# Kernel optimization log

Hardware: AMD Instinct MI355X
Metric: run time of the kernel (lower is better)

## Reference

```python
import jax, jax.numpy as jnp
import numpy as np
import math

NUM_HEADS = 16
SIZE = 1024
HEAD_SIZE = SIZE // NUM_HEADS
B, S = 2, 2048


def setup_inputs() -> dict:
    key = jax.random.key(0)
    ks = jax.random.split(key, 11)
    sc = 1.0 / math.sqrt(SIZE)
    inp = {
        "q": jax.random.normal(ks[0], (B, S, SIZE), dtype=jnp.float32),
        "k": jax.random.normal(ks[1], (B, S, SIZE), dtype=jnp.float32),
        "v": jax.random.normal(ks[2], (B, S, SIZE), dtype=jnp.float32),
        "Wq": jax.random.normal(ks[3], (SIZE, SIZE), dtype=jnp.float32) * sc,
        "bq": jax.random.normal(ks[4], (SIZE,), dtype=jnp.float32) * sc,
        "Wk": jax.random.normal(ks[5], (SIZE, SIZE), dtype=jnp.float32) * sc,
        "bk": jax.random.normal(ks[6], (SIZE,), dtype=jnp.float32) * sc,
        "Wv": jax.random.normal(ks[7], (SIZE, SIZE), dtype=jnp.float32) * sc,
        "bv": jax.random.normal(ks[8], (SIZE,), dtype=jnp.float32) * sc,
        "Wo": jax.random.normal(ks[9], (SIZE, SIZE), dtype=jnp.float32) * sc,
        "bo": jax.random.normal(ks[10], (SIZE,), dtype=jnp.float32) * sc,
    }
    return inp


def _split_heads(x):
    # [B, S, SIZE] -> [B, H, S, D]
    b, s, _ = x.shape
    return x.reshape(b, s, NUM_HEADS, HEAD_SIZE).transpose(0, 2, 1, 3)


def reference(q, k, v, Wq, bq, Wk, bk, Wv, bv, Wo, bo):
    qh = _split_heads(q @ Wq.T + bq) / math.sqrt(HEAD_SIZE)  # [B,H,S,D]
    kh = _split_heads(k @ Wk.T + bk)
    vh = _split_heads(v @ Wv.T + bv)
    scores = jnp.einsum("bhqd,bhkd->bhqk", qh, kh)  # [B,H,S,S]
    attn = jax.nn.softmax(scores, axis=-1)
    ctx = jnp.einsum("bhqk,bhkd->bhqd", attn, vh)  # [B,H,S,D]
    ctx = ctx.transpose(0, 2, 1, 3).reshape(q.shape[0], -1, SIZE)
    return ctx @ Wo.T + bo
```

## Files before the change

kernel.cpp:

```cpp
#include <hip/hip_runtime.h>
#include <hip/hip_bf16.h>

#define SIZE 1024
#define NH 16
#define HD 64
#define BB 2
#define SS 2048
#define MROWS (BB * SS)
#define QT 256
#define NQT (SS / QT)
#define NKT ((SS / 2) / 64)

using bf16 = __hip_bfloat16;
using frag16 = __attribute__((ext_vector_type(8))) short;
using f32x4 = __attribute__((ext_vector_type(4))) float;
typedef unsigned int u32;

__device__ __forceinline__ void glds16(const bf16* g, bf16* l) {
    __builtin_amdgcn_global_load_lds(
        (const __attribute__((address_space(1))) u32*)g,
        (__attribute__((address_space(3))) u32*)l, 16, 0, 0);
}

__device__ __forceinline__ void cvt_store8(bf16* dst, const float* src) {
    float4 a = *(const float4*)src;
    float4 b = *(const float4*)(src + 4);
    bf16 t[8];
    t[0] = __float2bfloat16(a.x); t[1] = __float2bfloat16(a.y);
    t[2] = __float2bfloat16(a.z); t[3] = __float2bfloat16(a.w);
    t[4] = __float2bfloat16(b.x); t[5] = __float2bfloat16(b.y);
    t[6] = __float2bfloat16(b.z); t[7] = __float2bfloat16(b.w);
    *(uint4*)dst = *(const uint4*)t;
}

__global__ __launch_bounds__(256) void cast_kernel(
    const float* __restrict__ Wq, const float* __restrict__ Wk,
    const float* __restrict__ Wv, const float* __restrict__ Wo,
    const float* __restrict__ q, const float* __restrict__ k,
    const float* __restrict__ v,
    bf16* __restrict__ Wb, bf16* __restrict__ qb,
    bf16* __restrict__ kb, bf16* __restrict__ vb)
{
    const size_t WN = (size_t)SIZE * SIZE;
    const size_t AN = (size_t)MROWS * SIZE;
    const size_t e = ((size_t)blockIdx.x * 256 + threadIdx.x) * 8;
    if (e < 4 * WN) {
        const int which = (int)(e >> 20);
        const size_t off = e & (WN - 1);
        const float* s = (which == 0) ? Wq : (which == 1) ? Wk : (which == 2) ? Wv : Wo;
        cvt_store8(Wb + e, s + off);
    } else {
        const size_t a = e - 4 * WN;
        const int which = (int)(a >> 22);
        const size_t off = a & (AN - 1);
        const float* s = (which == 0) ? q : (which == 1) ? k : v;
        bf16* d = (which == 0) ? qb : (which == 1) ? kb : vb;
        cvt_store8(d + off, s + off);
    }
}

__device__ __forceinline__ void gemm_body(
    const bf16* __restrict__ X, const bf16* __restrict__ W,
    const float* __restrict__ bias, bf16* __restrict__ Y, float scale, bool vt_mode,
    int bm, int bn)
{
    __shared__ __align__(16) bf16 smem[16384];
    bf16* As = smem;
    bf16* Bs = smem + 8192;

    const int tid = threadIdx.x;
    const int wave = tid >> 6;
    const int lane = tid & 63;
    const int lane15 = lane & 15;
    const int quad = lane >> 4;
    const int wm = (wave & 1) * 64;
    const int wn = (wave >> 1) * 64;

    f32x4 acc[4][4];
#pragma unroll
    for (int i = 0; i < 4; i++)
#pragma unroll
        for (int j = 0; j < 4; j++)
            acc[i][j] = (f32x4){0.f, 0.f, 0.f, 0.f};

    const int srow = lane >> 2;
    const int scol = (lane & 3) * 8;

#define STAGE(KT, BUF)                                                         \
    {                                                                          \
        _Pragma("unroll")                                                      \
        for (int n = 0; n < 2; n++) {                                          \
            const int c = wave * 2 + n;          \
            glds16(X + (size_t)(bm + c * 16 + srow) * SIZE + (KT) * 32 + scol, \
                   As + (BUF) * 4096 + c * 512);                               \
            glds16(W + (size_t)(bn + c * 16 + srow) * SIZE + (KT) * 32 + scol, \
                   Bs + (BUF) * 4096 + c * 512);                               \
        }                                                                      \
    }

    STAGE(0, 0);
    __syncthreads();

    for (int kt = 0; kt < SIZE / 32; kt++) {
        const int buf = kt & 1;
        if (kt + 1 < SIZE / 32) STAGE(kt + 1, buf ^ 1);
        __builtin_amdgcn_sched_barrier(0);

        frag16 a[4], b[4];
#pragma unroll
        for (int mi = 0; mi < 4; mi++)
            a[mi] = *(const frag16*)(As + buf * 4096 + (wm + mi * 16 + lane15) * 32 + quad * 8);
#pragma unroll
        for (int ni = 0; ni < 4; ni++)
            b[ni] = *(const frag16*)(Bs + buf * 4096 + (wn + ni * 16 + lane15) * 32 + quad * 8);
#pragma unroll
        for (int mi = 0; mi < 4; mi++)
#pragma unroll
            for (int ni = 0; ni < 4; ni++)
                acc[mi][ni] = __builtin_amdgcn_mfma_f32_16x16x32_bf16(
                    a[mi], b[ni], acc[mi][ni], 0, 0, 0);

        __syncthreads();
    }
#undef STAGE

    if (!vt_mode) {
#pragma unroll
        for (int ni = 0; ni < 4; ni++) {
            const int col = bn + wn + ni * 16 + lane15;
            const float bv = bias[col];
#pragma unroll
            for (int mi = 0; mi < 4; mi++) {
                const int row = bm + wm + mi * 16 + quad * 4;
#pragma unroll
                for (int r = 0; r < 4; r++)
                    Y[(size_t)(row + r) * SIZE + col] =
                        __float2bfloat16((acc[mi][ni][r] + bv) * scale);
            }
        }
    } else {
        bf16* tr = smem;
        const int bloc = bm >> 11;
        const int s0g = bm & (SS - 1);
#pragma unroll
        for (int p = 0; p < 2; p++) {
            __syncthreads();
            if ((wave >> 1) == p) {
#pragma unroll
                for (int ni = 0; ni < 4; ni++) {
                    const int colp = ni * 16 + lane15;
                    const float bv = bias[bn + p * 64 + colp];
#pragma unroll
                    for (int mi = 0; mi < 4; mi++) {
                        const int row = wm + mi * 16 + quad * 4;
#pragma unroll
                        for (int r = 0; r < 4; r++)
                            tr[colp * 136 + row + r] =
                                __float2bfloat16(acc[mi][ni][r] + bv);
                    }
                }
            }
            __syncthreads();
            const int colp = tid >> 2;
            const int gcol = bn + p * 64 + colp;
            const int hh = gcol >> 6, dd = gcol & (HD - 1);
            bf16* dst = (bf16*)Y + ((size_t)(bloc * NH + hh) * HD + dd) * SS
                        + s0g + (tid & 3) * 32;
            const bf16* src = tr + colp * 136 + (tid & 3) * 32;
#pragma unroll
            for (int j = 0; j < 4; j++)
                *(uint4*)(dst + j * 8) = *(const uint4*)(src + j * 8);
        }
    }
}

__global__ __launch_bounds__(256) void qkv_proj_kernel(
    const bf16* __restrict__ qb, const bf16* __restrict__ kb, const bf16* __restrict__ vb,
    const bf16* __restrict__ Wb,
    const float* __restrict__ bq, const float* __restrict__ bk, const float* __restrict__ bv,
    bf16* __restrict__ qh, bf16* __restrict__ kh, bf16* __restrict__ vt)
{
    const int f = blockIdx.x;
    const int w = (f & 7) * 96 + (f >> 3);
    const int z = w >> 8;
    const int rem = w & 255;
    const int bn = (rem & 7) * 128;
    const int bm = (rem >> 3) * 128;

    const bf16 *X, *W; const float* bi; bf16* Y; float sc; bool vm;
    if (z == 0)      { X = qb; W = Wb;                   bi = bq; Y = qh; sc = 0.125f; vm = false; }
    else if (z == 1) { X = kb; W = Wb + SIZE * SIZE;     bi = bk; Y = kh; sc = 1.0f;   vm = false; }
    else             { X = vb; W = Wb + 2 * SIZE * SIZE; bi = bv; Y = vt; sc = 1.0f;   vm = true;  }
    gemm_body(X, W, bi, Y, sc, vm, bm, bn);
}

__global__ __launch_bounds__(256) void attn_kernel(
    const bf16* __restrict__ qh, const bf16* __restrict__ kh,
    const bf16* __restrict__ vt, bf16* __restrict__ po, float* __restrict__ pl)
{
    __shared__ __align__(16) bf16 Ps[4][64][72];

    const int tid = threadIdx.x;
    const int wave = tid >> 6;
    const int lane = tid & 63;
    const int lane15 = lane & 15;
    const int quad = lane >> 4;

    const int f = blockIdx.x;
    const int w = (f & 7) * 64 + (f >> 3);
    const int bh = w >> 4;
    const int within = w & 15;
    const int b = bh >> 4;
    const int h = bh & 15;
    const int qt = within >> 1;
    const int sh = within & 1;
    const int q0 = qt * QT;

    const size_t baseq = (size_t)b * SS * SIZE + (size_t)h * HD;
    const size_t basev = (size_t)(b * NH + h) * HD * SS;
    const float LOG2E = 1.44269504088896340736f;
    const float OFF = 12.0f * LOG2E;

    frag16 aq[4][2];
#pragma unroll
    for (int m = 0; m < 4; m++) {
        const int qrow = q0 + wave * 64 + m * 16 + lane15;
        const bf16* qp = qh + baseq + (size_t)qrow * SIZE + quad * 8;
        aq[m][0] = *(const frag16*)(qp);
        aq[m][1] = *(const frag16*)(qp + 32);
    }

    frag16 bones;
#pragma unroll
    for (int e = 0; e < 8; e++) bones[e] = (short)0x3F80;

    f32x4 ofrag[4][4], l_frag[4];
#pragma unroll
    for (int m = 0; m < 4; m++) {
        l_frag[m] = (f32x4){0.f, 0.f, 0.f, 0.f};
#pragma unroll
        for (int dt = 0; dt < 4; dt++) ofrag[m][dt] = (f32x4){0.f, 0.f, 0.f, 0.f};
    }

    const bf16* kbase = kh + baseq + (size_t)(sh * (SS / 2) + lane15) * SIZE + quad * 8;
    const bf16* vbase = vt + basev + (size_t)lane15 * SS + sh * (SS / 2) + quad * 8;

    for (int kt = 0; kt < NKT; kt++) {
        const int s0 = kt * 64;

        frag16 kf[4][2], bv[4][2];
#pragma unroll
        for (int nt = 0; nt < 4; nt++) {
            const bf16* kp = kbase + (size_t)(s0 + nt * 16) * SIZE;
            kf[nt][0] = *(const frag16*)(kp);
            kf[nt][1] = *(const frag16*)(kp + 32);
        }
#pragma unroll
        for (int dt = 0; dt < 4; dt++) {
            const bf16* vp = vbase + (size_t)(dt * 16) * SS + s0;
            bv[dt][0] = *(const frag16*)(vp);
            bv[dt][1] = *(const frag16*)(vp + 32);
        }

#pragma unroll
        for (int m = 0; m < 4; m++) {
#pragma unroll
            for (int nt = 0; nt < 4; nt++) {
                f32x4 c = (f32x4){0.f, 0.f, 0.f, 0.f};
                c = __builtin_amdgcn_mfma_f32_16x16x32_bf16(kf[nt][0], aq[m][0], c, 0, 0, 0);
                c = __builtin_amdgcn_mfma_f32_16x16x32_bf16(kf[nt][1], aq[m][1], c, 0, 0, 0);
                bf16 p4[4];
#pragma unroll
                for (int r = 0; r < 4; r++)
                    p4[r] = __float2bfloat16(exp2f(c[r] * LOG2E - OFF));
                *(uint2*)&Ps[wave][m * 16 + lane15][nt * 16 + quad * 4] = *(const uint2*)p4;
            }
        }
        __builtin_amdgcn_wave_barrier();

        frag16 ap[4][2];
#pragma unroll
        for (int m = 0; m < 4; m++)
#pragma unroll
            for (int c2 = 0; c2 < 2; c2++)
                ap[m][c2] = *(const frag16*)&Ps[wave][m * 16 + lane15][c2 * 32 + quad * 8];

        __builtin_amdgcn_s_setprio(1);
#pragma unroll
        for (int m = 0; m < 4; m++)
#pragma unroll
            for (int c2 = 0; c2 < 2; c2++)
                l_frag[m] = __builtin_amdgcn_mfma_f32_16x16x32_bf16(
                    ap[m][c2], bones, l_frag[m], 0, 0, 0);

#pragma unroll
        for (int dt = 0; dt < 4; dt++) {
#pragma unroll
            for (int m = 0; m < 4; m++) {
                ofrag[m][dt] = __builtin_amdgcn_mfma_f32_16x16x32_bf16(ap[m][0], bv[dt][0], ofrag[m][dt], 0, 0, 0);
                ofrag[m][dt] = __builtin_amdgcn_mfma_f32_16x16x32_bf16(ap[m][1], bv[dt][1], ofrag[m][dt], 0, 0, 0);
            }
        }
        __builtin_amdgcn_s_setprio(0);
    }

    const int pb = ((b * NH + h) * NQT + qt) * 2 + sh;
    if (lane15 == 0) {
        float* plp = pl + (size_t)pb * QT;
#pragma unroll
        for (int m = 0; m < 4; m++)
#pragma unroll
            for (int r = 0; r < 4; r++)
                plp[wave * 64 + m * 16 + quad * 4 + r] = l_frag[m][r];
    }
    bf16* pop = po + (size_t)pb * QT * HD;
#pragma unroll
    for (int m = 0; m < 4; m++)
#pragma unroll
        for (int dt = 0; dt < 4; dt++)
#pragma unroll
            for (int r = 0; r < 4; r++)
                pop[(size_t)(wave * 64 + m * 16 + quad * 4 + r) * HD + dt * 16 + lane15] =
                    __float2bfloat16(ofrag[m][dt][r]);
}

__global__ __launch_bounds__(256) void out_proj_kernel(
    const bf16* __restrict__ po, const float* __restrict__ pl,
    const bf16* __restrict__ Wob, const float* __restrict__ bo,
    float* __restrict__ out)
{
    __shared__ __align__(16) bf16 As[2 * 64 * 32];
    __shared__ __align__(16) bf16 Bs[2 * 128 * 32];

    const int f = blockIdx.x;
    const int w = (f & 7) * 64 + (f >> 3);
    const int bn = (w & 7) * 128;
    const int bm = (w >> 3) * 64;

    const int tid = threadIdx.x;
    const int wave = tid >> 6;
    const int lane = tid & 63;
    const int lane15 = lane & 15;
    const int quad = lane >> 4;
    const int wn = wave * 32;

    f32x4 acc[4][2];
#pragma unroll
    for (int i = 0; i < 4; i++)
#pragma unroll
        for (int j = 0; j < 2; j++)
            acc[i][j] = (f32x4){0.f, 0.f, 0.f, 0.f};

    const int srow = lane >> 2;
    const int scol = (lane & 3) * 8;

    const int arow = tid >> 2;
    const int acol = (tid & 3) * 8;
    const int gr = bm + arow;
    const int bIdx = gr >> 11;
    const int s = gr & (SS - 1);
    const int qt8 = s >> 8;
    const int sq = s & (QT - 1);

    uint4 p0a, p1a, p0b, p1b;
    float l0, l1;

#define ALOAD(KT)                                                                 \
    {                                                                             \
        const int pb0_ = ((bIdx * NH + (KT)) * NQT + qt8) * 2;                    \
        const bf16* q0_ = po + (size_t)pb0_ * QT * HD + sq * HD;                  \
        const bf16* q1_ = po + (size_t)(pb0_ + 1) * QT * HD + sq * HD;            \
        p0a = *(const uint4*)(q0_ + acol);                                        \
        p0b = *(const uint4*)(q0_ + 32 + acol);                                   \
        p1a = *(const uint4*)(q1_ + acol);                                        \
        p1b = *(const uint4*)(q1_ + 32 + acol);                                   \
        l0 = pl[(size_t)pb0_ * QT + sq];                                          \
        l1 = pl[(size_t)(pb0_ + 1) * QT + sq];                                    \
    }

    ALOAD(0);

    for (int kt = 0; kt < NH; kt++) {
        __syncthreads();
        {
            const float inv = 1.0f / fmaxf(l0 + l1, 1e-30f);
            const bf16* x0 = (const bf16*)&p0a; const bf16* y0 = (const bf16*)&p1a;
            const bf16* x1 = (const bf16*)&p0b; const bf16* y1 = (const bf16*)&p1b;
            bf16 o0[8], o1[8];
#pragma unroll
            for (int e = 0; e < 8; e++) {
                o0[e] = __float2bfloat16((__bfloat162float(x0[e]) + __bfloat162float(y0[e])) * inv);
                o1[e] = __float2bfloat16((__bfloat162float(x1[e]) + __bfloat162float(y1[e])) * inv);
            }
            *(uint4*)(As + 0 * 2048 + arow * 32 + acol) = *(const uint4*)o0;
            *(uint4*)(As + 1 * 2048 + arow * 32 + acol) = *(const uint4*)o1;
        }
#pragma unroll
        for (int n = 0; n < 4; n++) {
            const int c = wave * 4 + n;
            const int plane = c >> 3;
            const int cc = c & 7;
            glds16(Wob + (size_t)(bn + cc * 16 + srow) * SIZE + kt * 64 + plane * 32 + scol,
                   Bs + c * 512);
        }
        __syncthreads();

        if (kt + 1 < NH) ALOAD(kt + 1);

#pragma unroll
        for (int kk = 0; kk < 2; kk++) {
            frag16 a[4], b[2];
#pragma unroll
            for (int mi = 0; mi < 4; mi++)
                a[mi] = *(const frag16*)(As + kk * 2048 + (mi * 16 + lane15) * 32 + quad * 8);
#pragma unroll
            for (int ni = 0; ni < 2; ni++)
                b[ni] = *(const frag16*)(Bs + kk * 4096 + (wn + ni * 16 + lane15) * 32 + quad * 8);
#pragma unroll
            for (int mi = 0; mi < 4; mi++)
#pragma unroll
                for (int ni = 0; ni < 2; ni++)
                    acc[mi][ni] = __builtin_amdgcn_mfma_f32_16x16x32_bf16(
                        a[mi], b[ni], acc[mi][ni], 0, 0, 0);
        }
    }
#undef ALOAD

#pragma unroll
    for (int ni = 0; ni < 2; ni++) {
        const int col = bn + wn + ni * 16 + lane15;
        const float bv = bo[col];
#pragma unroll
        for (int mi = 0; mi < 4; mi++) {
            const int row = bm + mi * 16 + quad * 4;
#pragma unroll
            for (int r = 0; r < 4; r++)
                out[(size_t)(row + r) * SIZE + col] = acc[mi][ni][r] + bv;
        }
    }
}

extern "C" void kernel_launch(void* const* d_in, const int* in_sizes, int n_in,
                              void* d_out, int out_size, void* d_ws, size_t ws_size,
                              hipStream_t stream) {
    const float* q  = (const float*)d_in[0];
    const float* k  = (const float*)d_in[1];
    const float* v  = (const float*)d_in[2];
    const float* Wq = (const float*)d_in[3];
    const float* bq = (const float*)d_in[4];
    const float* Wk = (const float*)d_in[5];
    const float* bk = (const float*)d_in[6];
    const float* Wv = (const float*)d_in[7];
    const float* bv = (const float*)d_in[8];
    const float* Wo = (const float*)d_in[9];
    const float* bo = (const float*)d_in[10];
    float* out = (float*)d_out;

    bf16* Wb  = (bf16*)d_ws;
    bf16* qb  = Wb + (size_t)4 * SIZE * SIZE;
    bf16* kb  = qb + (size_t)MROWS * SIZE;
    bf16* vb  = kb + (size_t)MROWS * SIZE;
    bf16* qh  = vb + (size_t)MROWS * SIZE;
    bf16* kh  = qh + (size_t)MROWS * SIZE;
    bf16* vt  = kh + (size_t)MROWS * SIZE;
    bf16* po  = qb;
    float* pl = (float*)Wb;

    cast_kernel<<<dim3(8192, 1, 1), 256, 0, stream>>>(
        Wq, Wk, Wv, Wo, q, k, v, Wb, qb, kb, vb);
    qkv_proj_kernel<<<dim3(768, 1, 1), 256, 0, stream>>>(
        qb, kb, vb, Wb, bq, bk, bv, qh, kh, vt);
    attn_kernel<<<dim3(512, 1, 1), 256, 0, stream>>>(qh, kh, vt, po, pl);
    out_proj_kernel<<<dim3(512, 1, 1), 256, 0, stream>>>(
        po, pl, Wb + (size_t)3 * SIZE * SIZE, bo, out);
}
```

Baseline: 255.9 us.

## Stage K tiles through double-buffered LDS with register prefetch in attention

Each of the four waves previously loaded the same K tile from global memory into registers on its own. The block now loads each K tile once cooperatively, prefetching the next tile into registers while the current one is computed, and commits it to a double-buffered LDS array after a block barrier. This removes redundant global K traffic and hides load latency. In exchange it adds a __syncthreads per iteration, extra LDS and register use, and a sched_barrier that constrains instruction scheduling.

```diff
diff --git a/kernel.cpp b/kernel.cpp
--- a/kernel.cpp
+++ b/kernel.cpp
@@ -198,6 +198,7 @@
     const bf16* __restrict__ qh, const bf16* __restrict__ kh,
     const bf16* __restrict__ vt, bf16* __restrict__ po, float* __restrict__ pl)
 {
+    __shared__ __align__(16) bf16 Ks[2][64][72];
     __shared__ __align__(16) bf16 Ps[4][64][72];
 
     const int tid = threadIdx.x;
@@ -242,26 +243,46 @@
         for (int dt = 0; dt < 4; dt++) ofrag[m][dt] = (f32x4){0.f, 0.f, 0.f, 0.f};
     }
 
-    const bf16* kbase = kh + baseq + (size_t)(sh * (SS / 2) + lane15) * SIZE + quad * 8;
+    const int sr = tid >> 3;
+    const int sc = (tid & 7) * 8;
+
     const bf16* vbase = vt + basev + (size_t)lane15 * SS + sh * (SS / 2) + quad * 8;
 
+    uint4 rk0, rk1;
+#define ISSUE_K(KT)                                                            \
+    {                                                                          \
+        const int s0_ = sh * (SS / 2) + (KT) * 64;                             \
+        rk0 = *(const uint4*)(kh + baseq + (size_t)(s0_ + sr) * SIZE + sc);    \
+        rk1 = *(const uint4*)(kh + baseq + (size_t)(s0_ + sr + 32) * SIZE + sc);\
+    }
+#define COMMIT_K(BUF)                                                          \
+    {                                                                          \
+        *(uint4*)&Ks[BUF][sr][sc] = rk0; *(uint4*)&Ks[BUF][sr + 32][sc] = rk1; \
+    }
+
+    ISSUE_K(0); COMMIT_K(0);
+    __syncthreads();
+
     for (int kt = 0; kt < NKT; kt++) {
+        const int buf = kt & 1;
         const int s0 = kt * 64;
-
-        frag16 kf[4][2], bv[4][2];
-#pragma unroll
-        for (int nt = 0; nt < 4; nt++) {
-            const bf16* kp = kbase + (size_t)(s0 + nt * 16) * SIZE;
-            kf[nt][0] = *(const frag16*)(kp);
-            kf[nt][1] = *(const frag16*)(kp + 32);
-        }
+        if (kt + 1 < NKT) ISSUE_K(kt + 1);
+
+        frag16 bv[4][2];
 #pragma unroll
         for (int dt = 0; dt < 4; dt++) {
             const bf16* vp = vbase + (size_t)(dt * 16) * SS + s0;
             bv[dt][0] = *(const frag16*)(vp);
             bv[dt][1] = *(const frag16*)(vp + 32);
         }
-
+        __builtin_amdgcn_sched_barrier(0);
+
+        frag16 kf[4][2];
+#pragma unroll
+        for (int nt = 0; nt < 4; nt++) {
+            kf[nt][0] = *(const frag16*)&Ks[buf][nt * 16 + lane15][quad * 8];
+            kf[nt][1] = *(const frag16*)&Ks[buf][nt * 16 + lane15][32 + quad * 8];
+        }
 #pragma unroll
         for (int m = 0; m < 4; m++) {
 #pragma unroll
@@ -302,7 +323,14 @@
             }
         }
         __builtin_amdgcn_s_setprio(0);
-    }
+
+        if (kt + 1 < NKT) {
+            COMMIT_K(buf ^ 1);
+            __syncthreads();
+        }
+    }
+#undef ISSUE_K
+#undef COMMIT_K
 
     const int pb = ((b * NH + h) * NQT + qt) * 2 + sh;
     if (lane15 == 0) {
```

Measured after the change: 253.6 us. Within noise of the previous version (-0.9%).
